# Performance work log

Measured on AMD Instinct MI355X. Metric: run time of the kernel, lower is better.

The kernel has to match this reference:

```python
import jax, jax.numpy as jnp
import numpy as np

B, T, C = 4, 4096, 256

def setup_inputs() -> dict:
    key = jax.random.key(0)
    ks = jax.random.split(key, 7)
    s = 1.0 / np.sqrt(C)
    return {
        "x": jax.random.normal(ks[0], (B, T, C), dtype=jnp.float32),
        "Wq": jax.random.uniform(ks[1], (C, C), jnp.float32, -s, s),
        "bq": jax.random.uniform(ks[2], (C,), jnp.float32, -s, s),
        "Wk": jax.random.uniform(ks[3], (C, C), jnp.float32, -s, s),
        "bk": jax.random.uniform(ks[4], (C,), jnp.float32, -s, s),
        "Wv": jax.random.uniform(ks[5], (C, C), jnp.float32, -s, s),
        "bv": jax.random.uniform(ks[6], (C,), jnp.float32, -s, s),
    }

def reference(x, Wq, bq, Wk, bk, Wv, bv):
    # Projections (torch Linear: y = x @ W^T + b; here W stored as [in,out])
    q = x @ Wq + bq  # [B,T,C]
    k = x @ Wk + bk
    v = x @ Wv + bv
    dk = q.shape[-1]
    scores = jnp.einsum('btc,bsc->bts', q, k) / jnp.sqrt(jnp.float32(dk))
    Tn = x.shape[1]
    causal = jnp.tril(jnp.ones((Tn, Tn), dtype=bool))  # [T,T]
    scores = jnp.where(causal[None, :, :], scores, jnp.float32(-1e9))
    attn = jax.nn.softmax(scores, axis=-1)
    return jnp.einsum('bts,bsc->btc', attn, v)
```

## Files before the change

### kernel.cpp

```cpp
#include <hip/hip_runtime.h>
#include <hip/hip_bf16.h>

#define T_SEQ 4096
#define DIM   256
#define NBATCH 4

typedef short s8v __attribute__((ext_vector_type(8)));
typedef float f4v __attribute__((ext_vector_type(4)));
typedef unsigned short u16;

#define MFMA16(a,b,c) __builtin_amdgcn_mfma_f32_16x16x32_bf16(a,b,c,0,0,0)
#define FENCE_LGKM() asm volatile("s_waitcnt lgkmcnt(0)" ::: "memory")

static __device__ __forceinline__ u16 f2bf(float f) {
  union { float f; unsigned int u; } c; c.f = f;
  unsigned int u = c.u;
  unsigned int r = (u + 0x7fffu + ((u >> 16) & 1u)) >> 16;
  return (u16)r;
}

static __device__ __forceinline__ s8v pack8(const float* p) {
  float4 a = *(const float4*)p;
  float4 b = *(const float4*)(p + 4);
  s8v r;
  r[0] = (short)f2bf(a.x); r[1] = (short)f2bf(a.y);
  r[2] = (short)f2bf(a.z); r[3] = (short)f2bf(a.w);
  r[4] = (short)f2bf(b.x); r[5] = (short)f2bf(b.y);
  r[6] = (short)f2bf(b.z); r[7] = (short)f2bf(b.w);
  return r;
}

__global__ void diag_fill_kernel(float* __restrict__ out, float val, int n) {
  int i = blockIdx.x * blockDim.x + threadIdx.x;
  if (i < n) out[i] = val;
}

__global__ void wtrans_kernel(const float* __restrict__ Wq, const float* __restrict__ Wk,
                              const float* __restrict__ Wv, u16* __restrict__ Wt) {
  __shared__ float tile[32][33];
  int m = blockIdx.z;
  const float* W = (m == 0) ? Wq : ((m == 1) ? Wk : Wv);
  int bx = blockIdx.x * 32, by = blockIdx.y * 32;
  int x = threadIdx.x, y = threadIdx.y;
  #pragma unroll
  for (int i = 0; i < 32; i += 8) tile[y + i][x] = W[(by + y + i) * DIM + bx + x];
  __syncthreads();
  u16* o = Wt + m * DIM * DIM;
  #pragma unroll
  for (int i = 0; i < 32; i += 8) o[(bx + y + i) * DIM + by + x] = f2bf(tile[x][y + i]);
}

__global__ __launch_bounds__(256) void proj_kernel(
    const float* __restrict__ x, const u16* __restrict__ Wt,
    const float* __restrict__ bk, const float* __restrict__ bv,
    u16* __restrict__ kf, u16* __restrict__ vf) {
  alignas(16) __shared__ u16 Kl[64 * 264];
  alignas(16) __shared__ u16 Vl[256 * 72];

  int bid = blockIdx.x;
  int which = blockIdx.y;
  int tid  = threadIdx.x;
  int wave = tid >> 6, lane = tid & 63, quad = lane >> 4, l16 = lane & 15;
  int row0 = bid * 64 + wave * 16;

  s8v a[8];
  const float* xp = x + (size_t)(row0 + l16) * DIM + quad * 8;
  #pragma unroll
  for (int ks = 0; ks < 8; ks++) a[ks] = pack8(xp + ks * 32);

  if (which == 0) {
    const u16* W = Wt + DIM * DIM;
    f4v acc[16];
    #pragma unroll
    for (int nt = 0; nt < 16; nt++) acc[nt] = (f4v){0.f, 0.f, 0.f, 0.f};
    #pragma unroll
    for (int ks = 0; ks < 8; ks++) {
      #pragma unroll
      for (int nt = 0; nt < 16; nt++) {
        s8v bfr = *(const s8v*)(W + (nt * 16 + l16) * DIM + ks * 32 + quad * 8);
        acc[nt] = MFMA16(a[ks], bfr, acc[nt]);
      }
    }
    #pragma unroll
    for (int nt = 0; nt < 16; nt++) {
      float bb = bk[nt * 16 + l16];
      #pragma unroll
      for (int r = 0; r < 4; r++)
        Kl[(wave * 16 + quad * 4 + r) * 264 + nt * 16 + l16] = f2bf(acc[nt][r] + bb);
    }
    __syncthreads();
    #pragma unroll
    for (int i = 0; i < 8; i++) {
      int o = tid + i * 256;
      int tile = o >> 10, rem = o & 1023;
      int f = rem >> 6, ln = rem & 63;
      int sl = tile * 32 + (f >> 3) * 16 + (ln & 15);
      int c  = (f & 7) * 32 + (ln >> 4) * 8;
      s8v v = *(const s8v*)&Kl[sl * 264 + c];
      *(s8v*)&kf[(((size_t)(bid * 2 + tile) * 16 + f) * 64 + ln) * 8] = v;
    }
  } else {
    const u16* W = Wt + 2 * DIM * DIM;
    f4v acc[16];
    #pragma unroll
    for (int nt = 0; nt < 16; nt++) acc[nt] = (f4v){0.f, 0.f, 0.f, 0.f};
    #pragma unroll
    for (int ks = 0; ks < 8; ks++) {
      #pragma unroll
      for (int nt = 0; nt < 16; nt++) {
        s8v bfr = *(const s8v*)(W + (nt * 16 + l16) * DIM + ks * 32 + quad * 8);
        acc[nt] = MFMA16(a[ks], bfr, acc[nt]);
      }
    }
    #pragma unroll
    for (int nt = 0; nt < 16; nt++) {
      float bb = bv[nt * 16 + l16];
      union { u16 h[4]; uint2 v2; } pk;
      #pragma unroll
      for (int r = 0; r < 4; r++) pk.h[r] = f2bf(acc[nt][r] + bb);
      *(uint2*)&Vl[(nt * 16 + l16) * 72 + wave * 16 + quad * 4] = pk.v2;
    }
    __syncthreads();
    #pragma unroll
    for (int i = 0; i < 8; i++) {
      int o = tid + i * 256;
      int tile = o >> 10, rem = o & 1023;
      int nt = rem >> 6, ln = rem & 63;
      int c  = nt * 16 + (ln & 15);
      int sl = tile * 32 + (ln >> 4) * 8;
      s8v v = *(const s8v*)&Vl[c * 72 + sl];
      *(s8v*)&vf[(((size_t)(bid * 2 + tile) * 16 + nt) * 64 + ln) * 8] = v;
    }
  }
}

__global__ __launch_bounds__(256, 2) void attn_kernel(
    const float* __restrict__ x, const u16* __restrict__ wtq, const float* __restrict__ bq,
    const u16* __restrict__ kf, const u16* __restrict__ vf, float* __restrict__ out) {
  alignas(16) __shared__ u16 QsObuf[16384];
  alignas(16) __shared__ u16 Ps[4 * 640];
  __shared__ float lbuf[32];

  int bid = blockIdx.x;
  int b   = bid & 3;
  int idx = (bid & 255) >> 2;
  int jt  = (bid < 256) ? idx : (127 - idx);
  int q0  = jt * 32;

  int tid = threadIdx.x;
  int wave = tid >> 6, lane = tid & 63, quad = lane >> 4, l16 = lane & 15;
  int slab = wave & 1, h = wave >> 1;
  int rowBase = q0 + slab * 16;

  int n = jt + 1, mid = (n + 1) >> 1;
  int kv0 = h ? mid : 0, kv1 = h ? n : mid;

  const u16* kfb = kf + (size_t)b * 128 * 8192;
  const u16* vfb = vf + (size_t)b * 128 * 8192;
  u16* Qs = QsObuf;
  float* Obuf = (float*)QsObuf;

  if (wave < 2) {
    s8v xa[8];
    const float* xp = x + (size_t)(b * T_SEQ + q0 + wave * 16 + l16) * DIM + quad * 8;
    #pragma unroll
    for (int ks = 0; ks < 8; ks++) xa[ks] = pack8(xp + ks * 32);
    f4v qacc[16];
    #pragma unroll
    for (int nt = 0; nt < 16; nt++) qacc[nt] = (f4v){0.f, 0.f, 0.f, 0.f};
    #pragma unroll
    for (int ks = 0; ks < 8; ks++) {
      #pragma unroll
      for (int nt = 0; nt < 16; nt++) {
        s8v bfr = *(const s8v*)(wtq + (nt * 16 + l16) * DIM + ks * 32 + quad * 8);
        qacc[nt] = MFMA16(xa[ks], bfr, qacc[nt]);
      }
    }
    #pragma unroll
    for (int nt = 0; nt < 16; nt++) {
      float bb = bq[nt * 16 + l16];
      #pragma unroll
      for (int r = 0; r < 4; r++)
        Qs[(wave * 16 + quad * 4 + r) * 256 + nt * 16 + l16] =
            f2bf((qacc[nt][r] + bb) * 0.0625f);
    }
  }
  __syncthreads();
  s8v qa[8];
  #pragma unroll
  for (int ks = 0; ks < 8; ks++)
    qa[ks] = *(const s8v*)&Qs[(slab * 16 + l16) * 256 + ks * 32 + quad * 8];
  __syncthreads();

  f4v o[16];
  #pragma unroll
  for (int nt = 0; nt < 16; nt++) o[nt] = (f4v){0.f, 0.f, 0.f, 0.f};
  float lrow[4] = {0.f, 0.f, 0.f, 0.f};

  s8v kfr[16];
  if (kv0 < kv1) {
    const u16* kt = kfb + (size_t)kv0 * 8192;
    #pragma unroll
    for (int f = 0; f < 16; f++) kfr[f] = *(const s8v*)(kt + (f * 64 + lane) * 8);
  }

  for (int kv = kv0; kv < kv1; kv++) {
    const u16* vt = vfb + (size_t)kv * 8192;
    s8v vfr[16];
    #pragma unroll
    for (int nt = 0; nt < 16; nt++) vfr[nt] = *(const s8v*)(vt + (nt * 64 + lane) * 8);

    f4v sc[2];
    #pragma unroll
    for (int nt = 0; nt < 2; nt++) {
      f4v c = (f4v){0.f, 0.f, 0.f, 0.f};
      #pragma unroll
      for (int ks = 0; ks < 8; ks++) c = MFMA16(qa[ks], kfr[nt * 8 + ks], c);
      sc[nt] = c;
    }

    if (kv + 1 < kv1) {
      const u16* kt = kfb + (size_t)(kv + 1) * 8192;
      #pragma unroll
      for (int f = 0; f < 16; f++) kfr[f] = *(const s8v*)(kt + (f * 64 + lane) * 8);
    }

    int s0 = kv * 32 + l16;
    #pragma unroll
    for (int r = 0; r < 4; r++) {
      int tq = rowBase + quad * 4 + r;
      float v0 = (s0 > tq)      ? -1e30f : sc[0][r];
      float v1 = (s0 + 16 > tq) ? -1e30f : sc[1][r];
      float p0 = __expf(v0);
      float p1 = __expf(v1);
      Ps[wave * 640 + (quad * 4 + r) * 40 + l16]      = f2bf(p0);
      Ps[wave * 640 + (quad * 4 + r) * 40 + 16 + l16] = f2bf(p1);
      lrow[r] += p0 + p1;
    }
    FENCE_LGKM();
    s8v pa = *(const s8v*)&Ps[wave * 640 + l16 * 40 + quad * 8];
    #pragma unroll
    for (int nt = 0; nt < 16; nt++) o[nt] = MFMA16(pa, vfr[nt], o[nt]);
  }

  #pragma unroll
  for (int r = 0; r < 4; r++) {
    #pragma unroll
    for (int d = 1; d < 16; d <<= 1) lrow[r] += __shfl_xor(lrow[r], d);
  }

  if (h == 0) {
    float* Ob = Obuf + slab * 4096;
    #pragma unroll
    for (int nt = 0; nt < 16; nt++) {
      #pragma unroll
      for (int r = 0; r < 4; r++)
        Ob[(quad * 4 + r) * 256 + nt * 16 + l16] = o[nt][r];
    }
    if (l16 == 0) {
      #pragma unroll
      for (int r = 0; r < 4; r++) lbuf[slab * 16 + quad * 4 + r] = lrow[r];
    }
  }
  __syncthreads();
  if (h == 1) {
    float* Ob = Obuf + slab * 4096;
    float inv[4];
    #pragma unroll
    for (int r = 0; r < 4; r++)
      inv[r] = 1.0f / (lbuf[slab * 16 + quad * 4 + r] + lrow[r]);
    #pragma unroll
    for (int nt = 0; nt < 16; nt++) {
      #pragma unroll
      for (int r = 0; r < 4; r++) {
        size_t row = (size_t)(b * T_SEQ + rowBase + quad * 4 + r);
        out[row * DIM + nt * 16 + l16] =
            (Ob[(quad * 4 + r) * 256 + nt * 16 + l16] + o[nt][r]) * inv[r];
      }
    }
  }
}

extern "C" void kernel_launch(void* const* d_in, const int* in_sizes, int n_in,
                              void* d_out, int out_size, void* d_ws, size_t ws_size,
                              hipStream_t stream) {
  const float* x  = (const float*)d_in[0];
  const float* Wq = (const float*)d_in[1];
  const float* bq = (const float*)d_in[2];
  const float* Wk = (const float*)d_in[3];
  const float* bk = (const float*)d_in[4];
  const float* Wv = (const float*)d_in[5];
  const float* bv = (const float*)d_in[6];

  const size_t NTD = (size_t)NBATCH * T_SEQ * DIM;
  const size_t WT_ELEMS = (size_t)3 * DIM * DIM;
  const size_t REQ_BYTES = (WT_ELEMS + 2 * NTD) * sizeof(u16);

  if (ws_size < REQ_BYTES) {
    float val = (float)(ws_size >> 20);
    diag_fill_kernel<<<(out_size + 255) / 256, 256, 0, stream>>>((float*)d_out, val, out_size);
    return;
  }

  u16* ws = (u16*)d_ws;
  u16* WT = ws;
  u16* Kf = ws + WT_ELEMS;
  u16* Vf = Kf + NTD;

  wtrans_kernel<<<dim3(8, 8, 3), dim3(32, 8, 1), 0, stream>>>(Wq, Wk, Wv, WT);
  proj_kernel<<<dim3(256, 2, 1), dim3(256, 1, 1), 0, stream>>>(x, WT, bk, bv, Kf, Vf);
  attn_kernel<<<dim3(512, 1, 1), dim3(256, 1, 1), 0, stream>>>(x, WT, bq, Kf, Vf, (float*)d_out);
}
```

Before: 210.1 us.

## Make attention kernel persistent with atomic task queue and 4-way KV split

```diff
diff --git a/kernel.cpp b/kernel.cpp
--- a/kernel.cpp
+++ b/kernel.cpp
@@ -11,6 +11,8 @@
 
 #define MFMA16(a,b,c) __builtin_amdgcn_mfma_f32_16x16x32_bf16(a,b,c,0,0,0)
 #define FENCE_LGKM() asm volatile("s_waitcnt lgkmcnt(0)" ::: "memory")
+
+__device__ int g_cnt[4];
 
 static __device__ __forceinline__ u16 f2bf(float f) {
   union { float f; unsigned int u; } c; c.f = f;
@@ -37,6 +39,9 @@
 
 __global__ void wtrans_kernel(const float* __restrict__ Wq, const float* __restrict__ Wk,
                               const float* __restrict__ Wv, u16* __restrict__ Wt) {
+  if (blockIdx.x == 0 && blockIdx.y == 0 && blockIdx.z == 0 &&
+      threadIdx.y == 0 && threadIdx.x < 4)
+    g_cnt[threadIdx.x] = 0;
   __shared__ float tile[32][33];
   int m = blockIdx.z;
   const float* W = (m == 0) ? Wq : ((m == 1) ? Wk : Wv);
@@ -134,149 +139,149 @@
   }
 }
 
-__global__ __launch_bounds__(256, 2) void attn_kernel(
+__global__ __launch_bounds__(256, 3) void attn_kernel(
     const float* __restrict__ x, const u16* __restrict__ wtq, const float* __restrict__ bq,
     const u16* __restrict__ kf, const u16* __restrict__ vf, float* __restrict__ out) {
-  alignas(16) __shared__ u16 QsObuf[16384];
+  alignas(16) __shared__ u16 Qs[16 * 264];
+  alignas(16) __shared__ float ObA[16 * 258];
+  alignas(16) __shared__ float ObB[16 * 258];
   alignas(16) __shared__ u16 Ps[4 * 640];
-  __shared__ float lbuf[32];
+  __shared__ float lbuf[4][16];
+  __shared__ int taskS;
 
   int bid = blockIdx.x;
-  int b   = bid & 3;
-  int idx = (bid & 255) >> 2;
-  int jt  = (bid < 256) ? idx : (127 - idx);
-  int q0  = jt * 32;
-
+  int b = bid & 3;
   int tid = threadIdx.x;
   int wave = tid >> 6, lane = tid & 63, quad = lane >> 4, l16 = lane & 15;
-  int slab = wave & 1, h = wave >> 1;
-  int rowBase = q0 + slab * 16;
-
-  int n = jt + 1, mid = (n + 1) >> 1;
-  int kv0 = h ? mid : 0, kv1 = h ? n : mid;
 
   const u16* kfb = kf + (size_t)b * 128 * 8192;
   const u16* vfb = vf + (size_t)b * 128 * 8192;
-  u16* Qs = QsObuf;
-  float* Obuf = (float*)QsObuf;
-
-  if (wave < 2) {
-    s8v xa[8];
-    const float* xp = x + (size_t)(b * T_SEQ + q0 + wave * 16 + l16) * DIM + quad * 8;
-    #pragma unroll
-    for (int ks = 0; ks < 8; ks++) xa[ks] = pack8(xp + ks * 32);
-    f4v qacc[16];
-    #pragma unroll
-    for (int nt = 0; nt < 16; nt++) qacc[nt] = (f4v){0.f, 0.f, 0.f, 0.f};
-    #pragma unroll
-    for (int ks = 0; ks < 8; ks++) {
+
+  for (;;) {
+    if (tid == 0) taskS = atomicAdd(&g_cnt[b], 1);
+    __syncthreads();
+    int t = taskS;
+    if (t >= 256) break;
+    int q = 255 - t;
+    int row0 = q * 16;
+
+    {
+      s8v xa[8];
+      const float* xp = x + (size_t)(b * T_SEQ + row0 + l16) * DIM + quad * 8;
+      #pragma unroll
+      for (int ks = 0; ks < 8; ks++) xa[ks] = pack8(xp + ks * 32);
+      f4v qacc[4];
+      #pragma unroll
+      for (int j = 0; j < 4; j++) qacc[j] = (f4v){0.f, 0.f, 0.f, 0.f};
+      #pragma unroll
+      for (int ks = 0; ks < 8; ks++) {
+        #pragma unroll
+        for (int j = 0; j < 4; j++) {
+          int nt = wave * 4 + j;
+          s8v bfr = *(const s8v*)(wtq + (nt * 16 + l16) * DIM + ks * 32 + quad * 8);
+          qacc[j] = MFMA16(xa[ks], bfr, qacc[j]);
+        }
+      }
+      #pragma unroll
+      for (int j = 0; j < 4; j++) {
+        int nt = wave * 4 + j;
+        float bb = bq[nt * 16 + l16];
+        #pragma unroll
+        for (int r = 0; r < 4; r++)
+          Qs[(quad * 4 + r) * 264 + nt * 16 + l16] =
+              f2bf((qacc[j][r] + bb) * 0.0625f);
+      }
+    }
+    __syncthreads();
+    s8v qa[8];
+    #pragma unroll
+    for (int ks = 0; ks < 8; ks++)
+      qa[ks] = *(const s8v*)&Qs[l16 * 264 + ks * 32 + quad * 8];
+
+    int n = (q >> 1) + 1;
+    int lo = (n * wave) >> 2, hi = (n * (wave + 1)) >> 2;
+
+    f4v o[16];
+    #pragma unroll
+    for (int nt = 0; nt < 16; nt++) o[nt] = (f4v){0.f, 0.f, 0.f, 0.f};
+    float lrow[4] = {0.f, 0.f, 0.f, 0.f};
+
+    #pragma unroll 1
+    for (int kv = lo; kv < hi; kv++) {
+      const u16* kt = kfb + (size_t)kv * 8192;
+      const u16* vt = vfb + (size_t)kv * 8192;
+      s8v kfr0[8], kfr1[8];
+      #pragma unroll
+      for (int f = 0; f < 8; f++) kfr0[f] = *(const s8v*)(kt + (f * 64 + lane) * 8);
+      #pragma unroll
+      for (int f = 0; f < 8; f++) kfr1[f] = *(const s8v*)(kt + ((8 + f) * 64 + lane) * 8);
+
+      f4v c0 = (f4v){0.f, 0.f, 0.f, 0.f}, c1 = (f4v){0.f, 0.f, 0.f, 0.f};
+      #pragma unroll
+      for (int ks = 0; ks < 8; ks++) c0 = MFMA16(qa[ks], kfr0[ks], c0);
+      s8v vfr0[8];
+      #pragma unroll
+      for (int f = 0; f < 8; f++) vfr0[f] = *(const s8v*)(vt + (f * 64 + lane) * 8);
+      #pragma unroll
+      for (int ks = 0; ks < 8; ks++) c1 = MFMA16(qa[ks], kfr1[ks], c1);
+      s8v vfr1[8];
+      #pragma unroll
+      for (int f = 0; f < 8; f++) vfr1[f] = *(const s8v*)(vt + ((8 + f) * 64 + lane) * 8);
+
+      int s0 = kv * 32 + l16;
+      #pragma unroll
+      for (int r = 0; r < 4; r++) {
+        int tq = row0 + quad * 4 + r;
+        float v0 = (s0 > tq)      ? -1e30f : c0[r];
+        float v1 = (s0 + 16 > tq) ? -1e30f : c1[r];
+        float p0 = __expf(v0);
+        float p1 = __expf(v1);
+        Ps[wave * 640 + (quad * 4 + r) * 40 + l16]      = f2bf(p0);
+        Ps[wave * 640 + (quad * 4 + r) * 40 + 16 + l16] = f2bf(p1);
+        lrow[r] += p0 + p1;
+      }
+      FENCE_LGKM();
+      s8v pa = *(const s8v*)&Ps[wave * 640 + l16 * 40 + quad * 8];
+      #pragma unroll
+      for (int nt = 0; nt < 8; nt++) o[nt] = MFMA16(pa, vfr0[nt], o[nt]);
+      #pragma unroll
+      for (int nt = 0; nt < 8; nt++) o[8 + nt] = MFMA16(pa, vfr1[nt], o[8 + nt]);
+    }
+
+    #pragma unroll
+    for (int r = 0; r < 4; r++) {
+      #pragma unroll
+      for (int d = 1; d < 16; d <<= 1) lrow[r] += __shfl_xor(lrow[r], d);
+    }
+    if (l16 == 0) {
+      #pragma unroll
+      for (int r = 0; r < 4; r++) lbuf[wave][quad * 4 + r] = lrow[r];
+    }
+
+    float* Obw = (wave & 1) ? ObB : ObA;
+    if (wave < 2) {
       #pragma unroll
       for (int nt = 0; nt < 16; nt++) {
-        s8v bfr = *(const s8v*)(wtq + (nt * 16 + l16) * DIM + ks * 32 + quad * 8);
-        qacc[nt] = MFMA16(xa[ks], bfr, qacc[nt]);
-      }
-    }
-    #pragma unroll
-    for (int nt = 0; nt < 16; nt++) {
-      float bb = bq[nt * 16 + l16];
-      #pragma unroll
-      for (int r = 0; r < 4; r++)
-        Qs[(wave * 16 + quad * 4 + r) * 256 + nt * 16 + l16] =
-            f2bf((qacc[nt][r] + bb) * 0.0625f);
-    }
-  }
-  __syncthreads();
-  s8v qa[8];
-  #pragma unroll
-  for (int ks = 0; ks < 8; ks++)
-    qa[ks] = *(const s8v*)&Qs[(slab * 16 + l16) * 256 + ks * 32 + quad * 8];
-  __syncthreads();
-
-  f4v o[16];
-  #pragma unroll
-  for (int nt = 0; nt < 16; nt++) o[nt] = (f4v){0.f, 0.f, 0.f, 0.f};
-  float lrow[4] = {0.f, 0.f, 0.f, 0.f};
-
-  s8v kfr[16];
-  if (kv0 < kv1) {
-    const u16* kt = kfb + (size_t)kv0 * 8192;
-    #pragma unroll
-    for (int f = 0; f < 16; f++) kfr[f] = *(const s8v*)(kt + (f * 64 + lane) * 8);
-  }
-
-  for (int kv = kv0; kv < kv1; kv++) {
-    const u16* vt = vfb + (size_t)kv * 8192;
-    s8v vfr[16];
-    #pragma unroll
-    for (int nt = 0; nt < 16; nt++) vfr[nt] = *(const s8v*)(vt + (nt * 64 + lane) * 8);
-
-    f4v sc[2];
-    #pragma unroll
-    for (int nt = 0; nt < 2; nt++) {
-      f4v c = (f4v){0.f, 0.f, 0.f, 0.f};
-      #pragma unroll
-      for (int ks = 0; ks < 8; ks++) c = MFMA16(qa[ks], kfr[nt * 8 + ks], c);
-      sc[nt] = c;
-    }
-
-    if (kv + 1 < kv1) {
-      const u16* kt = kfb + (size_t)(kv + 1) * 8192;
-      #pragma unroll
-      for (int f = 0; f < 16; f++) kfr[f] = *(const s8v*)(kt + (f * 64 + lane) * 8);
-    }
-
-    int s0 = kv * 32 + l16;
-    #pragma unroll
-    for (int r = 0; r < 4; r++) {
-      int tq = rowBase + quad * 4 + r;
-      float v0 = (s0 > tq)      ? -1e30f : sc[0][r];
-      float v1 = (s0 + 16 > tq) ? -1e30f : sc[1][r];
-      float p0 = __expf(v0);
-      float p1 = __expf(v1);
-      Ps[wave * 640 + (quad * 4 + r) * 40 + l16]      = f2bf(p0);
-      Ps[wave * 640 + (quad * 4 + r) * 40 + 16 + l16] = f2bf(p1);
-      lrow[r] += p0 + p1;
-    }
-    FENCE_LGKM();
-    s8v pa = *(const s8v*)&Ps[wave * 640 + l16 * 40 + quad * 8];
-    #pragma unroll
-    for (int nt = 0; nt < 16; nt++) o[nt] = MFMA16(pa, vfr[nt], o[nt]);
-  }
-
-  #pragma unroll
-  for (int r = 0; r < 4; r++) {
-    #pragma unroll
-    for (int d = 1; d < 16; d <<= 1) lrow[r] += __shfl_xor(lrow[r], d);
-  }
-
-  if (h == 0) {
-    float* Ob = Obuf + slab * 4096;
-    #pragma unroll
-    for (int nt = 0; nt < 16; nt++) {
-      #pragma unroll
-      for (int r = 0; r < 4; r++)
-        Ob[(quad * 4 + r) * 256 + nt * 16 + l16] = o[nt][r];
-    }
-    if (l16 == 0) {
-      #pragma unroll
-      for (int r = 0; r < 4; r++) lbuf[slab * 16 + quad * 4 + r] = lrow[r];
-    }
-  }
-  __syncthreads();
-  if (h == 1) {
-    float* Ob = Obuf + slab * 4096;
-    float inv[4];
-    #pragma unroll
-    for (int r = 0; r < 4; r++)
-      inv[r] = 1.0f / (lbuf[slab * 16 + quad * 4 + r] + lrow[r]);
-    #pragma unroll
-    for (int nt = 0; nt < 16; nt++) {
-      #pragma unroll
-      for (int r = 0; r < 4; r++) {
-        size_t row = (size_t)(b * T_SEQ + rowBase + quad * 4 + r);
-        out[row * DIM + nt * 16 + l16] =
-            (Ob[(quad * 4 + r) * 256 + nt * 16 + l16] + o[nt][r]) * inv[r];
-      }
+        #pragma unroll
+        for (int r = 0; r < 4; r++)
+          Obw[(quad * 4 + r) * 258 + nt * 16 + l16] = o[nt][r];
+      }
+    }
+    __syncthreads();
+    if (wave >= 2) {
+      #pragma unroll
+      for (int nt = 0; nt < 16; nt++) {
+        #pragma unroll
+        for (int r = 0; r < 4; r++)
+          Obw[(quad * 4 + r) * 258 + nt * 16 + l16] += o[nt][r];
+      }
+    }
+    __syncthreads();
+    #pragma unroll
+    for (int row = 0; row < 16; row++) {
+      float s = lbuf[0][row] + lbuf[1][row] + lbuf[2][row] + lbuf[3][row];
+      out[((size_t)(b * T_SEQ + row0 + row)) * DIM + tid] =
+          (ObA[row * 258 + tid] + ObB[row * 258 + tid]) * (1.0f / s);
     }
   }
 }
@@ -309,5 +314,5 @@
 
   wtrans_kernel<<<dim3(8, 8, 3), dim3(32, 8, 1), 0, stream>>>(Wq, Wk, Wv, WT);
   proj_kernel<<<dim3(256, 2, 1), dim3(256, 1, 1), 0, stream>>>(x, WT, bk, bv, Kf, Vf);
-  attn_kernel<<<dim3(512, 1, 1), dim3(256, 1, 1), 0, stream>>>(x, WT, bq, Kf, Vf, (float*)d_out);
-}
+  attn_kernel<<<dim3(768, 1, 1), dim3(256, 1, 1), 0, stream>>>(x, WT, bq, Kf, Vf, (float*)d_out);
+}
```

New measurement: 294.4 us. 1.4x slower.
